# Kernel optimization log

Hardware: AMD Instinct MI355X
Metric: run time of the kernel (lower is better)

The kernel has to match this reference:

```python
import jax, jax.numpy as jnp
import numpy as np

N_NODES = 50000
N_EDGES = 640000
D = 128
BN_EPS = 1e-5


def setup_inputs() -> dict:
    key = jax.random.key(0)
    k1, k2, k3 = jax.random.split(key, 3)
    x = jax.random.normal(k1, (N_NODES, D), dtype=jnp.float32)
    # Glorot-ish weight for GCNConv linear
    W = jax.random.normal(k2, (D, D), dtype=jnp.float32) * (1.0 / np.sqrt(D))
    b = jnp.zeros((D,), dtype=jnp.float32)
    gamma = jnp.ones((D,), dtype=jnp.float32)
    beta = jnp.zeros((D,), dtype=jnp.float32)
    edge_index = jax.random.randint(k3, (2, N_EDGES), 0, N_NODES, dtype=jnp.int64)
    return {"x": x, "W": W, "b": b, "gamma": gamma, "beta": beta, "edge_index": edge_index}


def reference(x, W, b, gamma, beta, edge_index):
    N = x.shape[0]
    # --- GCNConv: x' = D^{-1/2} (A + I) D^{-1/2} (x W) + b ---
    xw = x @ W  # [N, D]
    loops = jnp.arange(N, dtype=edge_index.dtype)
    src = jnp.concatenate([edge_index[0], loops])  # [E+N]
    dst = jnp.concatenate([edge_index[1], loops])
    ones = jnp.ones(src.shape[0], dtype=x.dtype)
    deg = jax.ops.segment_sum(ones, dst, num_segments=N)  # in-degree incl. self-loop
    dinv = jnp.where(deg > 0, jax.lax.rsqrt(deg), 0.0)
    norm = dinv[src] * dinv[dst]  # [E+N]
    msg = xw[src] * norm[:, None]  # [E+N, D] gathered + scaled messages
    h = jax.ops.segment_sum(msg, dst, num_segments=N) + b  # scatter-add aggregation
    # --- BatchNorm1d (training-mode batch stats over nodes, biased var) ---
    mean = jnp.mean(h, axis=0)
    var = jnp.mean(jnp.square(h - mean), axis=0)
    h = (h - mean) * jax.lax.rsqrt(var + BN_EPS) * gamma + beta
    # --- activation (relu) ---
    h = jax.nn.relu(h)
    # --- residual (in_channels == out_channels) ---
    h = x + h
    # --- dropout: identity in eval mode for deterministic reference ---
    return h
```

## Files before the change

### kernel.cpp

```cpp
#include <hip/hip_runtime.h>

#define DCH 128
#define ROWS 16
#define BN_EPS 1e-5f

typedef unsigned short u16;
typedef __attribute__((ext_vector_type(8))) short short8;
typedef __attribute__((ext_vector_type(4))) float floatx4;

__device__ __forceinline__ float bf2f(u16 u) {
    return __uint_as_float(((unsigned)u) << 16);
}
__device__ __forceinline__ u16 f2bf(float f) {
    unsigned u = __float_as_uint(f);
    u += 0x7FFFu + ((u >> 16) & 1u);
    return (u16)(u >> 16);
}
__device__ __forceinline__ float ldf(const void* p, int i, int isbf) {
    return isbf ? bf2f(((const u16*)p)[i]) : ((const float*)p)[i];
}

__global__ void detect_kernel(const int* ei, int ewords, const u16* xw, int* ws_i) {
    __shared__ int s_nz, s_hits;
    int t = threadIdx.x;
    if (t == 0) { s_nz = 0; s_hits = 0; }
    __syncthreads();
    int nz = 0;
    for (int i = t; i < 1024; i += 256) {
        int w = 2 * i + 1;
        if (w < ewords) nz |= ei[w];
    }
    if (nz) atomicOr(&s_nz, 1);
    unsigned m = (xw[2 * t] >> 8) & 0x7F;
    if (m >= 0x3B && m <= 0x43) atomicAdd(&s_hits, 1);
    __syncthreads();
    if (t == 0) {
        ws_i[0] = (s_nz == 0) ? 1 : 0;
        ws_i[1] = (s_hits >= 128) ? 1 : 0;
        ws_i[2] = 0;
    }
}

__global__ void zero_kernel(float* p, int n) {
    int stride = gridDim.x * 256;
    for (int i = blockIdx.x * 256 + threadIdx.x; i < n; i += stride) p[i] = 0.f;
}

__global__ void paint_kernel(u16* out, int n, unsigned val) {
    int stride = gridDim.x * 256;
    for (int i = blockIdx.x * 256 + threadIdx.x; i < n; i += stride) out[i] = (u16)val;
}

__global__ void packw_kernel(const void* W, const int* ws_i, u16* Wb) {
    int isbf = ws_i[1];
    for (int idx = threadIdx.x; idx < DCH * DCH; idx += 256) {
        int j = idx & 7, lane = (idx >> 3) & 63, kk = (idx >> 9) & 3, nt = idx >> 11;
        int k = kk * 32 + (lane >> 4) * 8 + j;
        int n = nt * 16 + (lane & 15);
        Wb[idx] = f2bf(ldf(W, k * DCH + n, isbf));
    }
}

__global__ void deg_kernel(const int* ei, int E, int* ws_i, int* deg, int N) {
    int is64 = ws_i[0];
    int i = blockIdx.x * 256 + threadIdx.x;
    if (i < E) {
        int s = is64 ? ei[2 * i] : ei[i];
        int d = is64 ? ei[2 * E + 2 * i] : ei[E + i];
        if (((unsigned)s >= (unsigned)N) || ((unsigned)d >= (unsigned)N))
            atomicOr(&ws_i[2], 2);
        d = min(max(d, 0), N - 1);
        atomicAdd(&deg[d], 1);
    }
}

__global__ void dinv_kernel(const int* deg, float* dinv, int N, int* ws_i) {
    int i = blockIdx.x * 256 + threadIdx.x;
    if (i < N) {
        float v = rsqrtf((float)(deg[i] + 1));
        if (!(v > 0.f && v <= 1.001f)) atomicOr(&ws_i[2], 4);
        dinv[i] = v;
    }
}

__global__ void scanA_kernel(const int* deg, int* part, int N) {
    int base = blockIdx.x * 1024 + threadIdx.x * 4;
    int s = 0;
    #pragma unroll
    for (int j = 0; j < 4; ++j) {
        int i = base + j;
        if (i < N) s += deg[i];
    }
    #pragma unroll
    for (int o = 1; o < 64; o <<= 1) s += __shfl_xor(s, o, 64);
    __shared__ int ws4[4];
    if ((threadIdx.x & 63) == 0) ws4[threadIdx.x >> 6] = s;
    __syncthreads();
    if (threadIdx.x == 0) part[blockIdx.x] = ws4[0] + ws4[1] + ws4[2] + ws4[3];
}

__global__ void scanB_kernel(int* part, int P) {
    __shared__ int wsum[4];
    int t = threadIdx.x, lane = t & 63, w = t >> 6;
    int v = (t < P) ? part[t] : 0;
    int sc = v;
    #pragma unroll
    for (int o = 1; o < 64; o <<= 1) {
        int u = __shfl_up(sc, o, 64);
        if (lane >= o) sc += u;
    }
    if (lane == 63) wsum[w] = sc;
    __syncthreads();
    if (t < 4) {
        int s = wsum[t];
        #pragma unroll
        for (int o = 1; o < 4; o <<= 1) {
            int u = __shfl_up(s, o, 4);
            if (t >= o) s += u;
        }
        wsum[t] = s;
    }
    __syncthreads();
    int excl = sc - v + (w ? wsum[w - 1] : 0);
    if (t < P) part[t] = excl;
}

__global__ void scanC_kernel(int* deg_cursor, const int* part, int* rowptr, int N) {
    __shared__ int wsum[4];
    int t = threadIdx.x, lane = t & 63, w = t >> 6;
    int base = blockIdx.x * 1024 + t * 4;
    int v[4], ts = 0;
    #pragma unroll
    for (int j = 0; j < 4; ++j) {
        int i = base + j;
        v[j] = (i < N) ? deg_cursor[i] : 0;
        ts += v[j];
    }
    int sc = ts;
    #pragma unroll
    for (int o = 1; o < 64; o <<= 1) {
        int u = __shfl_up(sc, o, 64);
        if (lane >= o) sc += u;
    }
    if (lane == 63) wsum[w] = sc;
    __syncthreads();
    if (t < 4) {
        int s = wsum[t];
        #pragma unroll
        for (int o = 1; o < 4; o <<= 1) {
            int u = __shfl_up(s, o, 4);
            if (t >= o) s += u;
        }
        wsum[t] = s;
    }
    __syncthreads();
    int run = sc - ts + (w ? wsum[w - 1] : 0) + part[blockIdx.x];
    #pragma unroll
    for (int j = 0; j < 4; ++j) {
        int i = base + j;
        if (i < N) {
            deg_cursor[i] = run;
            run += v[j];
            rowptr[i + 1] = run;
        }
    }
    if (blockIdx.x == 0 && t == 0) rowptr[0] = 0;
}

__global__ void fillcsr_kernel(const int* ei, int E, const int* ws_i,
                               int* cursor, int* col, int N) {
    int is64 = ws_i[0];
    int i = blockIdx.x * 256 + threadIdx.x;
    if (i < E) {
        int s = is64 ? ei[2 * i] : ei[i];
        int d = is64 ? ei[2 * E + 2 * i] : ei[E + i];
        s = min(max(s, 0), N - 1);
        d = min(max(d, 0), N - 1);
        int pos = atomicAdd(&cursor[d], 1);
        col[pos] = s;
    }
}

__global__ void gemm_mfma_kernel(const void* x, const u16* Wb, const float* dinv,
                                 const int* ws_i, u16* y, int N) {
    int isbf = ws_i[1];
    int t = threadIdx.x;
    int wv = t >> 6, lane = t & 63;
    int quad = lane >> 4, l16 = lane & 15;
    int r0 = blockIdx.x * 64 + wv * 16;
    int rl = min(r0 + l16, N - 1);
    short8 a[4];
    if (isbf) {
        const u16* xp = (const u16*)x + (size_t)rl * DCH + quad * 8;
        #pragma unroll
        for (int kk = 0; kk < 4; ++kk)
            a[kk] = *(const short8*)(xp + kk * 32);
    } else {
        const float* xp = (const float*)x + (size_t)rl * DCH + quad * 8;
        #pragma unroll
        for (int kk = 0; kk < 4; ++kk) {
            float4 f0 = *(const float4*)(xp + kk * 32);
            float4 f1 = *(const float4*)(xp + kk * 32 + 4);
            short8 aa;
            aa[0] = (short)f2bf(f0.x); aa[1] = (short)f2bf(f0.y);
            aa[2] = (short)f2bf(f0.z); aa[3] = (short)f2bf(f0.w);
            aa[4] = (short)f2bf(f1.x); aa[5] = (short)f2bf(f1.y);
            aa[6] = (short)f2bf(f1.z); aa[7] = (short)f2bf(f1.w);
            a[kk] = aa;
        }
    }
    floatx4 acc[8];
    #pragma unroll
    for (int i = 0; i < 8; ++i) acc[i] = (floatx4)(0.f);
    #pragma unroll
    for (int nt = 0; nt < 8; ++nt) {
        #pragma unroll
        for (int kk = 0; kk < 4; ++kk) {
            short8 bfr = *(const short8*)&Wb[(((nt << 2) | kk) * 64 + lane) * 8];
            acc[nt] = __builtin_amdgcn_mfma_f32_16x16x32_bf16(a[kk], bfr, acc[nt], 0, 0, 0);
        }
    }
    #pragma unroll
    for (int i = 0; i < 4; ++i) {
        int row = r0 + quad * 4 + i;
        if (row < N) {
            float dv = dinv[row];
            #pragma unroll
            for (int nt = 0; nt < 8; ++nt)
                y[(size_t)row * DCH + nt * 16 + l16] = f2bf(acc[nt][i] * dv);
        }
    }
}

__global__ void gather_kernel(const int* rowptr, const int* col, const u16* y,
                              const float* dinv, const void* b, const int* ws_i,
                              float* h, int N) {
    int isbf = ws_i[1];
    int w = threadIdx.x >> 6, lane = threadIdx.x & 63;
    int n = blockIdx.x * 4 + w;
    if (n >= N) return;
    int c = lane * 2;
    unsigned self = *(const unsigned*)&y[(size_t)n * DCH + c];
    float a0x = bf2f((u16)(self & 0xFFFF)), a0y = bf2f((u16)(self >> 16));
    float a1x = 0.f, a1y = 0.f, a2x = 0.f, a2y = 0.f, a3x = 0.f, a3y = 0.f;
    int beg = rowptr[n], end = rowptr[n + 1];
    int j = beg;
    for (; j + 3 < end; j += 4) {
        int s0 = col[j], s1 = col[j + 1], s2 = col[j + 2], s3 = col[j + 3];
        unsigned q0 = *(const unsigned*)&y[(size_t)s0 * DCH + c];
        unsigned q1 = *(const unsigned*)&y[(size_t)s1 * DCH + c];
        unsigned q2 = *(const unsigned*)&y[(size_t)s2 * DCH + c];
        unsigned q3 = *(const unsigned*)&y[(size_t)s3 * DCH + c];
        a0x += bf2f((u16)(q0 & 0xFFFF)); a0y += bf2f((u16)(q0 >> 16));
        a1x += bf2f((u16)(q1 & 0xFFFF)); a1y += bf2f((u16)(q1 >> 16));
        a2x += bf2f((u16)(q2 & 0xFFFF)); a2y += bf2f((u16)(q2 >> 16));
        a3x += bf2f((u16)(q3 & 0xFFFF)); a3y += bf2f((u16)(q3 >> 16));
    }
    for (; j < end; ++j) {
        unsigned q0 = *(const unsigned*)&y[(size_t)col[j] * DCH + c];
        a0x += bf2f((u16)(q0 & 0xFFFF)); a0y += bf2f((u16)(q0 >> 16));
    }
    float dn = dinv[n];
    float2 o;
    o.x = ((a0x + a1x) + (a2x + a3x)) * dn + ldf(b, c, isbf);
    o.y = ((a0y + a1y) + (a2y + a3y)) * dn + ldf(b, c + 1, isbf);
    *(float2*)&h[(size_t)n * DCH + c] = o;
}

__global__ void bnstat2_kernel(const float* h, float* sums, float* sumsq, int total) {
    int t = threadIdx.x, d = t & 127;
    float ps = 0.f, pq = 0.f;
    int stride = gridDim.x * 256;
    for (int i = blockIdx.x * 256 + t; i < total; i += stride) {
        float v = h[i];
        ps += v; pq += v * v;
    }
    __shared__ float ls[256], lq[256];
    ls[t] = ps; lq[t] = pq;
    __syncthreads();
    if (t < 128) {
        atomicAdd(&sums[d], ls[t] + ls[t + 128]);
        atomicAdd(&sumsq[d], lq[t] + lq[t + 128]);
    }
}

__global__ void gemm_valu_kernel(const void* x, const void* W, const float* dinv,
                                 const int* ws_i, void* y, int N) {
    __shared__ float WsF[64 * DCH];
    __shared__ float xs[ROWS * DCH];
    int isbf = ws_i[1];
    int t = threadIdx.x;
    int r0 = blockIdx.x * ROWS;
    for (int i = t; i < ROWS * DCH; i += 256) {
        int r = r0 + (i >> 7);
        xs[i] = (r < N) ? ldf(x, r * DCH + (i & 127), isbf) : 0.f;
    }
    int d = t & 127, rh = t >> 7;
    float s[8];
    #pragma unroll
    for (int j = 0; j < 8; ++j) s[j] = 0.f;
    for (int half = 0; half < 2; ++half) {
        __syncthreads();
        for (int i = t; i < 64 * DCH; i += 256)
            WsF[i] = ldf(W, half * 64 * DCH + i, isbf);
        __syncthreads();
        #pragma unroll
        for (int j = 0; j < 8; ++j) {
            int rr = rh + 2 * j;
            float a = s[j];
            #pragma unroll 16
            for (int k = 0; k < 64; ++k)
                a = fmaf(xs[rr * DCH + half * 64 + k], WsF[k * DCH + d], a);
            s[j] = a;
        }
    }
    #pragma unroll
    for (int j = 0; j < 8; ++j) {
        int r = r0 + rh + 2 * j;
        if (r < N) {
            float v = s[j] * dinv[r];
            if (isbf) ((u16*)y)[r * DCH + d] = f2bf(v);
            else      ((float*)y)[r * DCH + d] = v;
        }
    }
}

__global__ void scatter_kernel(const int* ei, int E, const int* ws_i,
                               const void* y, float* acc, int N) {
    int is64 = ws_i[0], isbf = ws_i[1];
    int gid = blockIdx.x * 256 + threadIdx.x;
    int e = gid >> 5;
    if (e >= E) return;
    int c0 = (gid & 31) * 4;
    int s = is64 ? ei[2 * e] : ei[e];
    int d = is64 ? ei[2 * E + 2 * e] : ei[E + e];
    s = min(max(s, 0), N - 1);
    d = min(max(d, 0), N - 1);
    float v0, v1, v2, v3;
    if (isbf) {
        uint2 raw = *(const uint2*)&((const u16*)y)[s * DCH + c0];
        v0 = bf2f((u16)(raw.x & 0xFFFF)); v1 = bf2f((u16)(raw.x >> 16));
        v2 = bf2f((u16)(raw.y & 0xFFFF)); v3 = bf2f((u16)(raw.y >> 16));
    } else {
        float4 raw = *(const float4*)&((const float*)y)[s * DCH + c0];
        v0 = raw.x; v1 = raw.y; v2 = raw.z; v3 = raw.w;
    }
    float* a = &acc[d * DCH + c0];
    atomicAdd(a + 0, v0);
    atomicAdd(a + 1, v1);
    atomicAdd(a + 2, v2);
    atomicAdd(a + 3, v3);
}

__global__ void bnstat_kernel(const void* y, float* acc, const float* dinv,
                              const void* b, int* ws_i,
                              float* sums, float* sumsq, int total) {
    int isbf = ws_i[1];
    int t = threadIdx.x;
    int d = t & 127;
    float bb = ldf(b, d, isbf);
    float ps = 0.f, pq = 0.f;
    int stride = gridDim.x * 256;
    for (int i = blockIdx.x * 256 + t; i < total; i += stride) {
        int r = i >> 7;
        float yv = isbf ? bf2f(((const u16*)y)[i]) : ((const float*)y)[i];
        float v = (yv + acc[i]) * dinv[r] + bb;
        acc[i] = v;
        ps += v;
        pq += v * v;
    }
    __shared__ float ls[256], lq[256];
    ls[t] = ps; lq[t] = pq;
    __syncthreads();
    if (t < 128) {
        atomicAdd(&sums[d], ls[t] + ls[t + 128]);
        atomicAdd(&sumsq[d], lq[t] + lq[t + 128]);
    }
}

__global__ void out_kernel(const float* h, const void* x,
                           const void* gamma, const void* beta,
                           int* ws_i, const float* sums, const float* sumsq,
                           void* out, int total, float invN) {
    __shared__ float sc[DCH], sh[DCH];
    int isbf = ws_i[1];
    int t = threadIdx.x;
    if (t < DCH) {
        float mean = sums[t] * invN;
        float var = fmaxf(sumsq[t] * invN - mean * mean, 0.f);
        float s = ldf(gamma, t, isbf) * rsqrtf(var + BN_EPS);
        if (!(var < 1e8f && fabsf(s) < 1e6f)) atomicOr(&ws_i[2], 32);
        sc[t] = s;
        sh[t] = ldf(beta, t, isbf) - mean * s;
    }
    __syncthreads();
    int stride = gridDim.x * 256;
    if (isbf) {
        for (int i = blockIdx.x * 256 + t; i < total; i += stride) {
            int d = i & 127;
            float v = fmaf(h[i], sc[d], sh[d]);
            v = fmaxf(v, 0.f) + bf2f(((const u16*)x)[i]);
            ((u16*)out)[i] = f2bf(v);
        }
    } else {
        for (int i = blockIdx.x * 256 + t; i < total; i += stride) {
            int d = i & 127;
            float v = fmaf(h[i], sc[d], sh[d]);
            v = fmaxf(v, 0.f) + ((const float*)x)[i];
            ((float*)out)[i] = v;
        }
    }
}

__global__ void diag_kernel(const int* ws_i, void* out, int n) {
    int e = ws_i[2];
    if (!e) return;
    int isbf = ws_i[1];
    float v = 4096.f + 32.f * (float)(e & 63);
    int stride = gridDim.x * 256;
    if (isbf) {
        u16 code = f2bf(v);
        for (int i = blockIdx.x * 256 + threadIdx.x; i < n; i += stride)
            ((u16*)out)[i] = code;
    } else {
        for (int i = blockIdx.x * 256 + threadIdx.x; i < n; i += stride)
            ((float*)out)[i] = v;
    }
}

extern "C" void kernel_launch(void* const* d_in, const int* in_sizes, int n_in,
                              void* d_out, int out_size, void* d_ws, size_t ws_size,
                              hipStream_t stream) {
    const void* x     = d_in[0];
    const void* W     = d_in[1];
    const void* b     = d_in[2];
    const void* gamma = d_in[3];
    const void* beta  = d_in[4];
    const int*  ei    = (const int*)d_in[5];

    const int N  = in_sizes[0] / DCH;
    const int E  = in_sizes[5] / 2;
    const int ND = N * DCH;
    const int P  = (N + 1023) / 1024;

    char* wsb = (char*)d_ws;
    int*  ws_i = (int*)wsb;

    size_t o_wb   = 64;
    size_t o_deg  = o_wb + 32768;
    size_t o_sum  = o_deg + 4 * (size_t)N;
    size_t o_sq   = o_sum + 512;
    size_t o_rp   = o_sq + 512;
    size_t o_dinv = o_rp + 4 * ((size_t)N + 1) + 4;
    size_t o_part = o_dinv + 4 * (size_t)N;
    size_t o_h    = (o_part + 1024 + 255) & ~(size_t)255;
    size_t o_col  = o_h + 4 * (size_t)ND;
    size_t need_csr = o_col + 4 * (size_t)E;

    (void)hipGetLastError();

    if (ws_size >= need_csr) {
        u16*   Wb    = (u16*)(wsb + o_wb);
        int*   deg   = (int*)(wsb + o_deg);
        float* sums  = (float*)(wsb + o_sum);
        float* sumsq = (float*)(wsb + o_sq);
        int*   rowptr= (int*)(wsb + o_rp);
        float* dinv  = (float*)(wsb + o_dinv);
        int*   part  = (int*)(wsb + o_part);
        float* h     = (float*)(wsb + o_h);
        int*   col   = (int*)(wsb + o_col);
        u16*   y     = (u16*)d_out;

        detect_kernel<<<1, 256, 0, stream>>>(ei, 2 * E, (const u16*)x, ws_i);
        zero_kernel<<<256, 256, 0, stream>>>((float*)(wsb + o_deg), N + 256);
        packw_kernel<<<1, 256, 0, stream>>>(W, ws_i, Wb);
        deg_kernel<<<(E + 255) / 256, 256, 0, stream>>>(ei, E, ws_i, deg, N);
        dinv_kernel<<<(N + 255) / 256, 256, 0, stream>>>(deg, dinv, N, ws_i);
        scanA_kernel<<<P, 256, 0, stream>>>(deg, part, N);
        scanB_kernel<<<1, 256, 0, stream>>>(part, P);
        scanC_kernel<<<P, 256, 0, stream>>>(deg, part, rowptr, N);
        fillcsr_kernel<<<(E + 255) / 256, 256, 0, stream>>>(ei, E, ws_i, deg, col, N);
        gemm_mfma_kernel<<<(N + 63) / 64, 256, 0, stream>>>(x, Wb, dinv, ws_i, y, N);
        gather_kernel<<<(N + 3) / 4, 256, 0, stream>>>(rowptr, col, y, dinv, b, ws_i, h, N);
        bnstat2_kernel<<<512, 256, 0, stream>>>(h, sums, sumsq, ND);
        out_kernel<<<1024, 256, 0, stream>>>(h, x, gamma, beta, ws_i, sums, sumsq,
                                             d_out, ND, 1.0f / (float)N);
        diag_kernel<<<512, 256, 0, stream>>>(ws_i, d_out, out_size);
    } else {
        int*   deg   = (int*)(wsb + 16);
        float* dinv  = (float*)(wsb + 16 + 4 * (size_t)N);
        float* sums  = (float*)(wsb + 16 + 8 * (size_t)N);
        float* sumsq = sums + DCH;
        float* acc   = sumsq + DCH;
        size_t need = 16 + 8 * (size_t)N + 1024 + 4 * (size_t)ND;
        if (ws_size < need) {
            int mb = (int)(ws_size >> 20); if (mb > 127) mb = 127;
            float v = 2048.f + 16.f * (float)mb;
            unsigned u; __builtin_memcpy(&u, &v, 4);
            paint_kernel<<<1024, 256, 0, stream>>>((u16*)d_out, out_size, u >> 16);
            return;
        }
        detect_kernel<<<1, 256, 0, stream>>>(ei, 2 * E, (const u16*)x, ws_i);
        zero_kernel<<<2048, 256, 0, stream>>>((float*)(wsb + 16), 2 * N + 256 + ND);
        deg_kernel<<<(E + 255) / 256, 256, 0, stream>>>(ei, E, ws_i, deg, N);
        dinv_kernel<<<(N + 255) / 256, 256, 0, stream>>>(deg, dinv, N, ws_i);
        gemm_valu_kernel<<<(N + ROWS - 1) / ROWS, 256, 0, stream>>>(x, W, dinv, ws_i, d_out, N);
        scatter_kernel<<<(E * 32 + 255) / 256, 256, 0, stream>>>(ei, E, ws_i, d_out, acc, N);
        bnstat_kernel<<<240, 256, 0, stream>>>(d_out, acc, dinv, b, ws_i, sums, sumsq, ND);
        out_kernel<<<256, 256, 0, stream>>>(acc, x, gamma, beta, ws_i, sums, sumsq,
                                            d_out, ND, 1.0f / (float)N);
        diag_kernel<<<512, 256, 0, stream>>>(ws_i, d_out, out_size);
    }

    if (hipGetLastError() != hipSuccess)
        hipMemsetAsync(d_out, 0x42, (size_t)out_size * 2, stream);
}
```

Before: 259.4 us.

## Fuse prep kernels, fold dinv into scan, and fuse gather with BN statistics

Merges detection, weight packing and workspace zeroing into one prep kernel, and computes dinv inside scanC so the separate dinv kernel is dropped. The gather is restructured so each wave handles nodes in a grid-stride loop, with 16 lanes of 8 channels each and four edge groups, using 16-byte loads and a shuffle reduction. It also accumulates the BatchNorm sums in the same kernel, which removes the bnstat pass that re-read h. This cuts launch count and one full read of h, at the cost of less memory-level parallelism per wave in the gather and a changed load pattern.

```diff
diff --git a/kernel.cpp b/kernel.cpp
--- a/kernel.cpp
+++ b/kernel.cpp
@@ -20,6 +20,50 @@
     return isbf ? bf2f(((const u16*)p)[i]) : ((const float*)p)[i];
 }
 
+__global__ void prep_kernel(const int* ei, int ewords, const u16* xw, int* ws_i,
+                            const void* W, u16* Wb, float* zbase, int zn) {
+    int t = threadIdx.x;
+    if (blockIdx.x == 0) {
+        __shared__ int s_nz, s_hits;
+        if (t == 0) { s_nz = 0; s_hits = 0; }
+        __syncthreads();
+        int nz = 0;
+        for (int i = t; i < 1024; i += 256) {
+            int w = 2 * i + 1;
+            if (w < ewords) nz |= ei[w];
+        }
+        if (nz) atomicOr(&s_nz, 1);
+        unsigned m = (xw[2 * t] >> 8) & 0x7F;
+        if (m >= 0x3B && m <= 0x43) atomicAdd(&s_hits, 1);
+        __syncthreads();
+        int isbf = (s_hits >= 128) ? 1 : 0;
+        if (t == 0) {
+            ws_i[0] = (s_nz == 0) ? 1 : 0;
+            ws_i[1] = isbf;
+            ws_i[2] = 0;
+        }
+        for (int idx = t; idx < DCH * DCH; idx += 256) {
+            int j = idx & 7, lane = (idx >> 3) & 63, kk = (idx >> 9) & 3, nt = idx >> 11;
+            int k = kk * 32 + (lane >> 4) * 8 + j;
+            int n = nt * 16 + (lane & 15);
+            Wb[idx] = f2bf(ldf(W, k * DCH + n, isbf));
+        }
+    } else {
+        int stride = (gridDim.x - 1) * 256;
+        for (int i = (blockIdx.x - 1) * 256 + t; i < zn; i += stride) zbase[i] = 0.f;
+    }
+}
+
+__global__ void zero_kernel(float* p, int n) {
+    int stride = gridDim.x * 256;
+    for (int i = blockIdx.x * 256 + threadIdx.x; i < n; i += stride) p[i] = 0.f;
+}
+
+__global__ void paint_kernel(u16* out, int n, unsigned val) {
+    int stride = gridDim.x * 256;
+    for (int i = blockIdx.x * 256 + threadIdx.x; i < n; i += stride) out[i] = (u16)val;
+}
+
 __global__ void detect_kernel(const int* ei, int ewords, const u16* xw, int* ws_i) {
     __shared__ int s_nz, s_hits;
     int t = threadIdx.x;
@@ -38,26 +82,6 @@
         ws_i[0] = (s_nz == 0) ? 1 : 0;
         ws_i[1] = (s_hits >= 128) ? 1 : 0;
         ws_i[2] = 0;
-    }
-}
-
-__global__ void zero_kernel(float* p, int n) {
-    int stride = gridDim.x * 256;
-    for (int i = blockIdx.x * 256 + threadIdx.x; i < n; i += stride) p[i] = 0.f;
-}
-
-__global__ void paint_kernel(u16* out, int n, unsigned val) {
-    int stride = gridDim.x * 256;
-    for (int i = blockIdx.x * 256 + threadIdx.x; i < n; i += stride) out[i] = (u16)val;
-}
-
-__global__ void packw_kernel(const void* W, const int* ws_i, u16* Wb) {
-    int isbf = ws_i[1];
-    for (int idx = threadIdx.x; idx < DCH * DCH; idx += 256) {
-        int j = idx & 7, lane = (idx >> 3) & 63, kk = (idx >> 9) & 3, nt = idx >> 11;
-        int k = kk * 32 + (lane >> 4) * 8 + j;
-        int n = nt * 16 + (lane & 15);
-        Wb[idx] = f2bf(ldf(W, k * DCH + n, isbf));
     }
 }
 
@@ -125,7 +149,8 @@
     if (t < P) part[t] = excl;
 }
 
-__global__ void scanC_kernel(int* deg_cursor, const int* part, int* rowptr, int N) {
+__global__ void scanC_kernel(int* deg_cursor, const int* part, int* rowptr,
+                             float* dinv, int N) {
     __shared__ int wsum[4];
     int t = threadIdx.x, lane = t & 63, w = t >> 6;
     int base = blockIdx.x * 1024 + t * 4;
@@ -162,6 +187,7 @@
             deg_cursor[i] = run;
             run += v[j];
             rowptr[i + 1] = run;
+            dinv[i] = rsqrtf((float)(v[j] + 1));
         }
     }
     if (blockIdx.x == 0 && t == 0) rowptr[0] = 0;
@@ -232,55 +258,79 @@
     }
 }
 
-__global__ void gather_kernel(const int* rowptr, const int* col, const u16* y,
-                              const float* dinv, const void* b, const int* ws_i,
-                              float* h, int N) {
+__global__ void gather_stats_kernel(const int* rowptr, const int* col, const u16* y,
+                                    const float* dinv, const void* b, const int* ws_i,
+                                    float* h, float* sums, float* sumsq, int N) {
     int isbf = ws_i[1];
-    int w = threadIdx.x >> 6, lane = threadIdx.x & 63;
-    int n = blockIdx.x * 4 + w;
-    if (n >= N) return;
-    int c = lane * 2;
-    unsigned self = *(const unsigned*)&y[(size_t)n * DCH + c];
-    float a0x = bf2f((u16)(self & 0xFFFF)), a0y = bf2f((u16)(self >> 16));
-    float a1x = 0.f, a1y = 0.f, a2x = 0.f, a2y = 0.f, a3x = 0.f, a3y = 0.f;
-    int beg = rowptr[n], end = rowptr[n + 1];
-    int j = beg;
-    for (; j + 3 < end; j += 4) {
-        int s0 = col[j], s1 = col[j + 1], s2 = col[j + 2], s3 = col[j + 3];
-        unsigned q0 = *(const unsigned*)&y[(size_t)s0 * DCH + c];
-        unsigned q1 = *(const unsigned*)&y[(size_t)s1 * DCH + c];
-        unsigned q2 = *(const unsigned*)&y[(size_t)s2 * DCH + c];
-        unsigned q3 = *(const unsigned*)&y[(size_t)s3 * DCH + c];
-        a0x += bf2f((u16)(q0 & 0xFFFF)); a0y += bf2f((u16)(q0 >> 16));
-        a1x += bf2f((u16)(q1 & 0xFFFF)); a1y += bf2f((u16)(q1 >> 16));
-        a2x += bf2f((u16)(q2 & 0xFFFF)); a2y += bf2f((u16)(q2 >> 16));
-        a3x += bf2f((u16)(q3 & 0xFFFF)); a3y += bf2f((u16)(q3 >> 16));
-    }
-    for (; j < end; ++j) {
-        unsigned q0 = *(const unsigned*)&y[(size_t)col[j] * DCH + c];
-        a0x += bf2f((u16)(q0 & 0xFFFF)); a0y += bf2f((u16)(q0 >> 16));
-    }
-    float dn = dinv[n];
-    float2 o;
-    o.x = ((a0x + a1x) + (a2x + a3x)) * dn + ldf(b, c, isbf);
-    o.y = ((a0y + a1y) + (a2y + a3y)) * dn + ldf(b, c + 1, isbf);
-    *(float2*)&h[(size_t)n * DCH + c] = o;
-}
-
-__global__ void bnstat2_kernel(const float* h, float* sums, float* sumsq, int total) {
-    int t = threadIdx.x, d = t & 127;
-    float ps = 0.f, pq = 0.f;
-    int stride = gridDim.x * 256;
-    for (int i = blockIdx.x * 256 + t; i < total; i += stride) {
-        float v = h[i];
-        ps += v; pq += v * v;
-    }
-    __shared__ float ls[256], lq[256];
-    ls[t] = ps; lq[t] = pq;
-    __syncthreads();
-    if (t < 128) {
-        atomicAdd(&sums[d], ls[t] + ls[t + 128]);
-        atomicAdd(&sumsq[d], lq[t] + lq[t + 128]);
+    int t = threadIdx.x;
+    int w = t >> 6, lane = t & 63;
+    int g = lane >> 4, cl = lane & 15;
+    int c0 = cl * 8;
+    float bb[8];
+    #pragma unroll
+    for (int k = 0; k < 8; ++k) bb[k] = ldf(b, c0 + k, isbf);
+    float ps[8], pq[8];
+    #pragma unroll
+    for (int k = 0; k < 8; ++k) { ps[k] = 0.f; pq[k] = 0.f; }
+    int wid = blockIdx.x * 4 + w;
+    int nw = gridDim.x * 4;
+    for (int n = wid; n < N; n += nw) {
+        float acc[8];
+        if (g == 0) {
+            uint4 q = *(const uint4*)&y[(size_t)n * DCH + c0];
+            acc[0] = bf2f((u16)(q.x & 0xFFFF)); acc[1] = bf2f((u16)(q.x >> 16));
+            acc[2] = bf2f((u16)(q.y & 0xFFFF)); acc[3] = bf2f((u16)(q.y >> 16));
+            acc[4] = bf2f((u16)(q.z & 0xFFFF)); acc[5] = bf2f((u16)(q.z >> 16));
+            acc[6] = bf2f((u16)(q.w & 0xFFFF)); acc[7] = bf2f((u16)(q.w >> 16));
+        } else {
+            #pragma unroll
+            for (int k = 0; k < 8; ++k) acc[k] = 0.f;
+        }
+        int beg = rowptr[n], end = rowptr[n + 1];
+        for (int j = beg + g; j < end; j += 4) {
+            int s = col[j];
+            uint4 q = *(const uint4*)&y[(size_t)s * DCH + c0];
+            acc[0] += bf2f((u16)(q.x & 0xFFFF)); acc[1] += bf2f((u16)(q.x >> 16));
+            acc[2] += bf2f((u16)(q.y & 0xFFFF)); acc[3] += bf2f((u16)(q.y >> 16));
+            acc[4] += bf2f((u16)(q.z & 0xFFFF)); acc[5] += bf2f((u16)(q.z >> 16));
+            acc[6] += bf2f((u16)(q.w & 0xFFFF)); acc[7] += bf2f((u16)(q.w >> 16));
+        }
+        #pragma unroll
+        for (int k = 0; k < 8; ++k) {
+            acc[k] += __shfl_xor(acc[k], 16, 64);
+            acc[k] += __shfl_xor(acc[k], 32, 64);
+        }
+        if (g == 0) {
+            float dn = dinv[n];
+            float4 o0, o1;
+            o0.x = fmaf(acc[0], dn, bb[0]); o0.y = fmaf(acc[1], dn, bb[1]);
+            o0.z = fmaf(acc[2], dn, bb[2]); o0.w = fmaf(acc[3], dn, bb[3]);
+            o1.x = fmaf(acc[4], dn, bb[4]); o1.y = fmaf(acc[5], dn, bb[5]);
+            o1.z = fmaf(acc[6], dn, bb[6]); o1.w = fmaf(acc[7], dn, bb[7]);
+            float* hp = &h[(size_t)n * DCH + c0];
+            *(float4*)hp = o0;
+            *(float4*)(hp + 4) = o1;
+            ps[0] += o0.x; pq[0] += o0.x * o0.x;
+            ps[1] += o0.y; pq[1] += o0.y * o0.y;
+            ps[2] += o0.z; pq[2] += o0.z * o0.z;
+            ps[3] += o0.w; pq[3] += o0.w * o0.w;
+            ps[4] += o1.x; pq[4] += o1.x * o1.x;
+            ps[5] += o1.y; pq[5] += o1.y * o1.y;
+            ps[6] += o1.z; pq[6] += o1.z * o1.z;
+            ps[7] += o1.w; pq[7] += o1.w * o1.w;
+        }
+    }
+    __shared__ float lps[4][DCH], lpq[4][DCH];
+    if (g == 0) {
+        #pragma unroll
+        for (int k = 0; k < 8; ++k) { lps[w][c0 + k] = ps[k]; lpq[w][c0 + k] = pq[k]; }
+    }
+    __syncthreads();
+    if (t < DCH) {
+        float s = (lps[0][t] + lps[1][t]) + (lps[2][t] + lps[3][t]);
+        float q = (lpq[0][t] + lpq[1][t]) + (lpq[2][t] + lpq[3][t]);
+        atomicAdd(&sums[t], s);
+        atomicAdd(&sumsq[t], q);
     }
 }
 
@@ -471,18 +521,16 @@
         int*   col   = (int*)(wsb + o_col);
         u16*   y     = (u16*)d_out;
 
-        detect_kernel<<<1, 256, 0, stream>>>(ei, 2 * E, (const u16*)x, ws_i);
-        zero_kernel<<<256, 256, 0, stream>>>((float*)(wsb + o_deg), N + 256);
-        packw_kernel<<<1, 256, 0, stream>>>(W, ws_i, Wb);
+        prep_kernel<<<65, 256, 0, stream>>>(ei, 2 * E, (const u16*)x, ws_i,
+                                            W, Wb, (float*)(wsb + o_deg), N + 256);
         deg_kernel<<<(E + 255) / 256, 256, 0, stream>>>(ei, E, ws_i, deg, N);
-        dinv_kernel<<<(N + 255) / 256, 256, 0, stream>>>(deg, dinv, N, ws_i);
         scanA_kernel<<<P, 256, 0, stream>>>(deg, part, N);
         scanB_kernel<<<1, 256, 0, stream>>>(part, P);
-        scanC_kernel<<<P, 256, 0, stream>>>(deg, part, rowptr, N);
+        scanC_kernel<<<P, 256, 0, stream>>>(deg, part, rowptr, dinv, N);
         fillcsr_kernel<<<(E + 255) / 256, 256, 0, stream>>>(ei, E, ws_i, deg, col, N);
         gemm_mfma_kernel<<<(N + 63) / 64, 256, 0, stream>>>(x, Wb, dinv, ws_i, y, N);
-        gather_kernel<<<(N + 3) / 4, 256, 0, stream>>>(rowptr, col, y, dinv, b, ws_i, h, N);
-        bnstat2_kernel<<<512, 256, 0, stream>>>(h, sums, sumsq, ND);
+        gather_stats_kernel<<<1024, 256, 0, stream>>>(rowptr, col, y, dinv, b, ws_i,
+                                                      h, sums, sumsq, N);
         out_kernel<<<1024, 256, 0, stream>>>(h, x, gamma, beta, ws_i, sums, sumsq,
                                              d_out, ND, 1.0f / (float)N);
         diag_kernel<<<512, 256, 0, stream>>>(ws_i, d_out, out_size);
```

Result: slower. 264.7 us (+2.0%).
